# Kernel optimization log

Measured on AMD Instinct MI355X. Metric: run time of the kernel, lower is better.

## Reference

```python
import jax, jax.numpy as jnp
import numpy as np

REPEAT_STEP = 4  # speculative_num_draft_tokens


def setup_inputs() -> dict:
    key = jax.random.key(0)
    k1, k2, k3, k4, k5 = jax.random.split(key, 5)
    BS = 512
    M = BS * REPEAT_STEP          # 2048 expanded rows
    LEN_A = 16384
    LEN_B = 128
    LEN_OUT = LEN_A + LEN_B
    return {
        "page_table_dst": jax.random.randint(k1, (M, LEN_OUT), 0, 1000000, dtype=jnp.int32),
        "page_table_a": jax.random.randint(k2, (BS, LEN_A), 0, 1000000, dtype=jnp.int32),
        "page_table_b": jax.random.randint(k3, (M, LEN_B), 0, 1000000, dtype=jnp.int32),
        "seq_len_a": jax.random.randint(k4, (BS,), 0, LEN_A, dtype=jnp.int32),
        "seq_len_b": jax.random.randint(k5, (M,), 0, LEN_B, dtype=jnp.int32),
    }


def reference(page_table_dst, page_table_a, page_table_b, seq_len_a, seq_len_b):
    M, LEN_OUT = page_table_dst.shape
    LEN_A = page_table_a.shape[1]
    LEN_B = page_table_b.shape[1]

    idx_a = jnp.arange(M) // REPEAT_STEP            # [M] map expanded row -> base row
    sa = seq_len_a[idx_a][:, None]                  # [M,1]
    sb = seq_len_b[:, None]                         # [M,1]
    offs = jnp.arange(LEN_OUT)[None, :]             # [1,LEN_OUT]

    # source-A values: gather the base row, valid where offs < seq_len_a (and in bounds)
    a_rows = page_table_a[idx_a]                    # [M, LEN_A]
    a_idx = jnp.broadcast_to(jnp.clip(offs, 0, LEN_A - 1), (M, LEN_OUT))
    a_val = jnp.take_along_axis(a_rows, a_idx, axis=1)
    a_val = jnp.where((offs < sa) & (offs < LEN_A), a_val, 0)

    # source-B values: shifted by seq_len_a per row
    b_offs = offs - sa                              # [M,LEN_OUT]
    b_idx = jnp.clip(b_offs, 0, LEN_B - 1)
    b_val = jnp.take_along_axis(page_table_b, b_idx, axis=1)
    b_val = jnp.where((b_offs >= 0) & (b_offs < sb) & (b_offs < LEN_B), b_val, 0)

    spliced = jnp.where(offs < sa, a_val, b_val)
    total = sa + sb
    # positions beyond total_len keep the original dst contents (kernel masks stores)
    return jnp.where(offs < total, spliced, page_table_dst)
```

## Files before the change

### kernel.cpp

```cpp
#include <hip/hip_runtime.h>


__global__ __launch_bounds__(256) void splice_kernel(
    const int* __restrict__ dst,
    const int* __restrict__ a,
    const int* __restrict__ b,
    const int* __restrict__ seq_a,
    const int* __restrict__ seq_b,
    int* __restrict__ out,
    int LEN_OUT, int LEN_A, int LEN_B, int repeat_shift)
{
    const int m  = blockIdx.y;
    const int vc = blockIdx.x * blockDim.x + threadIdx.x;
    const int nvec = LEN_OUT >> 2;
    if (vc >= nvec) return;

    const int ia    = m >> repeat_shift;
    const int sa    = seq_a[ia];
    const int sb    = seq_b[m];
    const int total = sa + sb;
    const int j0    = vc << 2;

    const int* a_row   = a   + (size_t)ia * LEN_A;
    const int* dst_row = dst + (size_t)m  * LEN_OUT;

    int4 v;
    if (j0 + 3 < sa) {
        v = *(const int4*)(a_row + j0);
    } else if (j0 >= total) {
        v = *(const int4*)(dst_row + j0);
    } else {
        const int* b_row = b + (size_t)m * LEN_B;
        int vals[4];
#pragma unroll
        for (int k = 0; k < 4; ++k) {
            const int j = j0 + k;
            int val;
            if (j < sa)         val = a_row[j];
            else if (j < total) val = b_row[j - sa];
            else                val = dst_row[j];
            vals[k] = val;
        }
        v = make_int4(vals[0], vals[1], vals[2], vals[3]);
    }
    *(int4*)(out + (size_t)m * LEN_OUT + j0) = v;
}

extern "C" void kernel_launch(void* const* d_in, const int* in_sizes, int n_in,
                              void* d_out, int out_size, void* d_ws, size_t ws_size,
                              hipStream_t stream) {
    const int* dst   = (const int*)d_in[0];
    const int* a     = (const int*)d_in[1];
    const int* b     = (const int*)d_in[2];
    const int* seq_a = (const int*)d_in[3];
    const int* seq_b = (const int*)d_in[4];
    int* out = (int*)d_out;

    const int BS      = in_sizes[3];
    const int M       = in_sizes[4];
    const int LEN_A   = in_sizes[1] / BS;
    const int LEN_B   = in_sizes[2] / M;
    const int LEN_OUT = in_sizes[0] / M;
    const int repeat  = M / BS;
    int repeat_shift = 0;
    while ((1 << repeat_shift) < repeat) ++repeat_shift;

    const int nvec = LEN_OUT / 4;
    dim3 block(256);
    dim3 grid((nvec + 255) / 256, M);
    splice_kernel<<<grid, block, 0, stream>>>(dst, a, b, seq_a, seq_b, out,
                                              LEN_OUT, LEN_A, LEN_B, repeat_shift);
}
```

Baseline: 247.0 us.

## Process one base row per block with per-repeat teams and nontemporal streaming

```diff
diff --git a/kernel.cpp b/kernel.cpp
--- a/kernel.cpp
+++ b/kernel.cpp
@@ -1,49 +1,65 @@
 #include <hip/hip_runtime.h>
 
 
-__global__ __launch_bounds__(256) void splice_kernel(
+typedef int v4i __attribute__((ext_vector_type(4)));
+
+__global__ __launch_bounds__(1024) void splice_kernel(
     const int* __restrict__ dst,
     const int* __restrict__ a,
     const int* __restrict__ b,
     const int* __restrict__ seq_a,
     const int* __restrict__ seq_b,
     int* __restrict__ out,
-    int LEN_OUT, int LEN_A, int LEN_B, int repeat_shift)
+    int LEN_OUT, int LEN_A, int LEN_B, int repeat)
 {
-    const int m  = blockIdx.y;
-    const int vc = blockIdx.x * blockDim.x + threadIdx.x;
-    const int nvec = LEN_OUT >> 2;
-    if (vc >= nvec) return;
+    const int g    = blockIdx.x;
+    const int team = threadIdx.x >> 8;
+    const int tid  = threadIdx.x & 255;
+    const int m    = g * repeat + team;
 
-    const int ia    = m >> repeat_shift;
-    const int sa    = seq_a[ia];
+    const int sa    = seq_a[g];
     const int sb    = seq_b[m];
     const int total = sa + sb;
-    const int j0    = vc << 2;
 
-    const int* a_row   = a   + (size_t)ia * LEN_A;
-    const int* dst_row = dst + (size_t)m  * LEN_OUT;
+    const int NV = LEN_OUT >> 2;
+    const int nA = sa >> 2;
+    const int nT = (total + 3) >> 2;
 
-    int4 v;
-    if (j0 + 3 < sa) {
-        v = *(const int4*)(a_row + j0);
-    } else if (j0 >= total) {
-        v = *(const int4*)(dst_row + j0);
-    } else {
-        const int* b_row = b + (size_t)m * LEN_B;
-        int vals[4];
+    const int* a_row = a   + (size_t)g * LEN_A;
+    const int* d_row = dst + (size_t)m * LEN_OUT;
+    const int* b_row = b   + (size_t)m * LEN_B;
+    int*       o_row = out + (size_t)m * LEN_OUT;
+
+    const v4i* a4 = (const v4i*)a_row;
+    const v4i* d4 = (const v4i*)d_row;
+    v4i*       o4 = (v4i*)o_row;
+
+#pragma unroll 4
+    for (int vc = tid; vc < nA; vc += 256) {
+        v4i v = a4[vc];
+        __builtin_nontemporal_store(v, &o4[vc]);
+    }
+
+#pragma unroll 4
+    for (int vc = nT + tid; vc < NV; vc += 256) {
+        v4i v = __builtin_nontemporal_load(&d4[vc]);
+        __builtin_nontemporal_store(v, &o4[vc]);
+    }
+
+    for (int vc = nA + tid; vc < nT; vc += 256) {
+        const int j0 = vc << 2;
+        v4i v;
 #pragma unroll
         for (int k = 0; k < 4; ++k) {
             const int j = j0 + k;
             int val;
             if (j < sa)         val = a_row[j];
             else if (j < total) val = b_row[j - sa];
-            else                val = dst_row[j];
-            vals[k] = val;
+            else                val = d_row[j];
+            v[k] = val;
         }
-        v = make_int4(vals[0], vals[1], vals[2], vals[3]);
+        __builtin_nontemporal_store(v, &o4[vc]);
     }
-    *(int4*)(out + (size_t)m * LEN_OUT + j0) = v;
 }
 
 extern "C" void kernel_launch(void* const* d_in, const int* in_sizes, int n_in,
@@ -62,12 +78,9 @@
     const int LEN_B   = in_sizes[2] / M;
     const int LEN_OUT = in_sizes[0] / M;
     const int repeat  = M / BS;
-    int repeat_shift = 0;
-    while ((1 << repeat_shift) < repeat) ++repeat_shift;
 
-    const int nvec = LEN_OUT / 4;
-    dim3 block(256);
-    dim3 grid((nvec + 255) / 256, M);
+    dim3 block(256 * repeat);
+    dim3 grid(BS);
     splice_kernel<<<grid, block, 0, stream>>>(dst, a, b, seq_a, seq_b, out,
-                                              LEN_OUT, LEN_A, LEN_B, repeat_shift);
+                                              LEN_OUT, LEN_A, LEN_B, repeat);
 }
```

Result: no change. 250.8 us (+1.5%).
